# Performance work log

Hardware: AMD Instinct MI355X
Metric: run time of the kernel (lower is better)

Reference implementation:

```python
import jax, jax.numpy as jnp
import numpy as np

NUM_NODES = 64      # nodes per graph (fixed, required by flatten/matricize)
B = 256             # number of graphs
N = B * NUM_NODES   # total nodes
DEG = 16            # out-degree per node
E = N * DEG         # total edges
IN_C, OUT_C, HEADS, EDGE_DIM = 128, 64, 4, 16
NEG_SLOPE = 0.2     # PyG GATv2 leaky_relu slope


def setup_inputs() -> dict:
    key = jax.random.key(0)
    ks = jax.random.split(key, 10)
    x = jax.random.normal(ks[0], (N, IN_C), jnp.float32)
    # within-graph random edges: each node has DEG incoming edges
    dst = jnp.repeat(jnp.arange(N), DEG)
    src = (dst // NUM_NODES) * NUM_NODES + jax.random.randint(ks[1], (E,), 0, NUM_NODES)
    edge_index = jnp.stack([src, dst]).astype(jnp.int64)
    edge_attr = jax.random.normal(ks[2], (E, EDGE_DIM), jnp.float32)
    batch = (jnp.arange(N) // NUM_NODES).astype(jnp.int64)
    s = 0.1
    W_l = jax.random.normal(ks[3], (IN_C, HEADS * OUT_C), jnp.float32) * s
    W_r = jax.random.normal(ks[4], (IN_C, HEADS * OUT_C), jnp.float32) * s
    W_e = jax.random.normal(ks[5], (EDGE_DIM, HEADS * OUT_C), jnp.float32) * s
    att = jax.random.normal(ks[6], (HEADS, OUT_C), jnp.float32) * s
    b_gat = jax.random.normal(ks[7], (HEADS * OUT_C,), jnp.float32) * s
    lin_W = jax.random.normal(ks[8], (NUM_NODES * HEADS * OUT_C, NUM_NODES * OUT_C), jnp.float32) * 0.02
    lin_b = jax.random.normal(ks[9], (NUM_NODES * OUT_C,), jnp.float32) * 0.02
    return {"x": x, "edge_index": edge_index, "edge_attr": edge_attr, "batch": batch,
            "W_l": W_l, "W_r": W_r, "W_e": W_e, "att": att, "b_gat": b_gat,
            "lin_W": lin_W, "lin_b": lin_b}


def _gatv2(x, edge_index, edge_attr, W_l, W_r, W_e, att, b_gat):
    n = x.shape[0]
    src, dst = edge_index[0], edge_index[1]
    # add self loops (PyG default), edge_attr fill_value='mean'
    loop = jnp.arange(n)
    src = jnp.concatenate([src, loop])
    dst = jnp.concatenate([dst, loop])
    mean_ea = jnp.broadcast_to(edge_attr.mean(0, keepdims=True), (n, edge_attr.shape[1]))
    ea = jnp.concatenate([edge_attr, mean_ea], axis=0)
    H, C = att.shape
    xl = (x @ W_l).reshape(n, H, C)   # source transform
    xr = (x @ W_r).reshape(n, H, C)   # target transform
    ee = (ea @ W_e).reshape(-1, H, C)
    feat = xl[src] + xr[dst] + ee                              # [E+N, H, C]
    logits = jnp.einsum('ehc,hc->eh', jax.nn.leaky_relu(feat, NEG_SLOPE), att)
    # segment softmax over incoming edges of each dst node
    seg_max = jax.ops.segment_max(logits, dst, num_segments=n)
    ex = jnp.exp(logits - seg_max[dst])
    denom = jax.ops.segment_sum(ex, dst, num_segments=n)
    alpha = ex / denom[dst]                                    # [E+N, H]
    msg = alpha[:, :, None] * xl[src]                          # [E+N, H, C]
    summed = jax.ops.segment_sum(msg, dst, num_segments=n)
    # aggr='mean': average the weighted messages over neighbors
    cnt = jax.ops.segment_sum(jnp.ones((dst.shape[0],), x.dtype), dst, num_segments=n)
    out = summed / cnt[:, None, None]
    return out.reshape(n, H * C) + b_gat


def reference(x, edge_index, edge_attr, batch, W_l, W_r, W_e, att, b_gat, lin_W, lin_b):
    h = _gatv2(x, edge_index, edge_attr, W_l, W_r, W_e, att, b_gat)  # [N, H*C]
    # flatten: [B, num_nodes*H*C] (batch is sorted, fixed nodes per graph)
    h = h.reshape(B, NUM_NODES * HEADS * OUT_C)
    y = h @ lin_W + lin_b                                            # [B, num_nodes*C]
    # matricize back to node-major layout
    return y.reshape(-1, OUT_C)                                      # [N, C]
```

## Files before the change

### kernel.cpp

```cpp
#include <hip/hip_runtime.h>
#include <hip/hip_bf16.h>

#define N_NODES   16384
#define DEG       16
#define EDGES     262144
#define HC        256
#define KDIM      16384
#define NEG_SLOPE 0.2f

typedef __attribute__((ext_vector_type(8))) short short8;
typedef __attribute__((ext_vector_type(4))) float floatx4;

static __device__ __forceinline__ unsigned short f2bf(float f) {
    union { __hip_bfloat16 h; unsigned short u; } c;
    c.h = __float2bfloat16(f);
    return c.u;
}
static __device__ __forceinline__ unsigned int packbf2(float lo, float hi) {
    union { __hip_bfloat162 h2; unsigned int u; } c;
    c.h2 = __float22bfloat162_rn(make_float2(lo, hi));
    return c.u;
}

template <int CTRL>
static __device__ __forceinline__ float dpp_add(float v) {
    int x = __builtin_amdgcn_update_dpp(0, __float_as_int(v), CTRL, 0xF, 0xF, true);
    return v + __int_as_float(x);
}

__global__ __launch_bounds__(256) void k_ea_part(const float* __restrict__ ea,
                                                 float* __restrict__ part) {
    __shared__ float s[256];
    int b = blockIdx.x, t = threadIdx.x;
    int col = t & 15, r0 = t >> 4;
    const float* base = ea + (size_t)b * 1024 * 16;
    float acc = 0.f;
    for (int r = r0; r < 1024; r += 16) acc += base[r * 16 + col];
    s[t] = acc; __syncthreads();
    for (int off = 128; off >= 16; off >>= 1) {
        if (t < off) s[t] += s[t + off];
        __syncthreads();
    }
    if (t < 16) part[b * 16 + t] = s[t];
}

__global__ __launch_bounds__(256, 4) void k_attn(const int* __restrict__ ei,
                                                 const float* __restrict__ ea,
                                                 const float* __restrict__ eapart,
                                                 const float* __restrict__ att,
                                                 const float* __restrict__ We,
                                                 const float* __restrict__ x,
                                                 const float* __restrict__ Wl,
                                                 const float* __restrict__ Wr,
                                                 const float* __restrict__ bg,
                                                 unsigned short* __restrict__ hb) {
    __shared__ float xlS[64][68];
    __shared__ float xrS[64][68];
    __shared__ __align__(16) char uni[5376];
    __shared__ float mean[16];
    __shared__ float eeselfS[64];

    float* lgS = (float*)uni;
    unsigned int* srcSu = (unsigned int*)(uni + 4352);
    unsigned int* BsU = (unsigned int*)uni;
    float (*ps)[16] = (float(*)[16])uni;

    int t = threadIdx.x;
    int g = blockIdx.x & 255, h = blockIdx.x >> 8;
    int hc0 = h * 64;

    int wave = t >> 6, lane = t & 63;
    int q = lane >> 4, l15 = lane & 15, lk = lane >> 4;

    {
        int col = t & 15, bgi = t >> 4;
        float a = 0.f;
        #pragma unroll
        for (int i = 0; i < 16; ++i)
            a += eapart[(bgi + i * 16) * 16 + col];
        ps[bgi][col] = a;
        __syncthreads();
        if (t < 16) {
            float m = 0.f;
            #pragma unroll
            for (int i = 0; i < 16; ++i) m += ps[i][t];
            mean[t] = m * (1.f / (float)EDGES);
        }
        __syncthreads();
        if (t < 64) {
            float acc = 0.f;
            #pragma unroll
            for (int d = 0; d < 16; ++d) acc += mean[d] * We[d * 256 + hc0 + t];
            eeselfS[t] = acc;
        }
        __syncthreads();
    }

    {
        int wm = wave;
        const float* xrow = x + ((size_t)(g * 64 + wm * 16 + l15)) * 128 + lk * 8;
        floatx4 accL[4], accR[4];
        #pragma unroll
        for (int i = 0; i < 4; ++i) { accL[i] = (floatx4)(0.f); accR[i] = (floatx4)(0.f); }

        int bkp = t >> 4, bc4 = t & 15;

        for (int k0 = 0; k0 < 128; k0 += 32) {
            float4 xv0 = *(const float4*)(xrow + k0);
            float4 xv1 = *(const float4*)(xrow + k0 + 4);
            union { unsigned int u[4]; short8 v; } aa;
            aa.u[0] = packbf2(xv0.x, xv0.y);
            aa.u[1] = packbf2(xv0.z, xv0.w);
            aa.u[2] = packbf2(xv1.x, xv1.y);
            aa.u[3] = packbf2(xv1.z, xv1.w);
            short8 af = aa.v;

            #pragma unroll
            for (int side = 0; side < 2; ++side) {
                const float* Wsel = side ? Wr : Wl;
                __syncthreads();
                {
                    const float* wp = Wsel + (size_t)(k0 + 2 * bkp) * 256 + hc0 + bc4 * 4;
                    float4 r0 = *(const float4*)wp;
                    float4 r1 = *(const float4*)(wp + 256);
                    BsU[(bc4 * 4 + 0) * 18 + bkp] = packbf2(r0.x, r1.x);
                    BsU[(bc4 * 4 + 1) * 18 + bkp] = packbf2(r0.y, r1.y);
                    BsU[(bc4 * 4 + 2) * 18 + bkp] = packbf2(r0.z, r1.z);
                    BsU[(bc4 * 4 + 3) * 18 + bkp] = packbf2(r0.w, r1.w);
                }
                __syncthreads();
                #pragma unroll
                for (int ni = 0; ni < 4; ++ni) {
                    int nr = ni * 16 + l15;
                    union { uint2 u[2]; short8 v; } bb;
                    bb.u[0] = *(const uint2*)&BsU[nr * 18 + lk * 4];
                    bb.u[1] = *(const uint2*)&BsU[nr * 18 + lk * 4 + 2];
                    if (side == 0)
                        accL[ni] = __builtin_amdgcn_mfma_f32_16x16x32_bf16(af, bb.v, accL[ni], 0, 0, 0);
                    else
                        accR[ni] = __builtin_amdgcn_mfma_f32_16x16x32_bf16(af, bb.v, accR[ni], 0, 0, 0);
                }
            }
        }
        #pragma unroll
        for (int ni = 0; ni < 4; ++ni) {
            #pragma unroll
            for (int r = 0; r < 4; ++r) {
                int node = wm * 16 + lk * 4 + r;
                xlS[node][l15 * 4 + ni] = accL[ni][r];
                xrS[node][l15 * 4 + ni] = accR[ni][r];
            }
        }
    }
    __syncthreads();

    {
        int4 v = *(const int4*)(ei + (size_t)g * 1024 + t * 4);
        srcSu[t] = (unsigned int)(v.x & 63) | ((unsigned int)(v.y & 63) << 8) |
                   ((unsigned int)(v.z & 63) << 16) | ((unsigned int)(v.w & 63) << 24);
    }

    short8 wf[4];
    float  attv[4];
    #pragma unroll
    for (int nt = 0; nt < 4; ++nt) {
        attv[nt] = att[hc0 + nt * 16 + l15];
        if (q < 2) {
            const float* wp = We + (size_t)(q * 8) * 256 + hc0 + nt * 16 + l15;
            float w0 = wp[0*256], w1 = wp[1*256], w2 = wp[2*256], w3 = wp[3*256];
            float w4 = wp[4*256], w5 = wp[5*256], w6 = wp[6*256], w7 = wp[7*256];
            union { unsigned int u[4]; short8 v; } bb;
            bb.u[0] = packbf2(w0, w1);
            bb.u[1] = packbf2(w2, w3);
            bb.u[2] = packbf2(w4, w5);
            bb.u[3] = packbf2(w6, w7);
            wf[nt] = bb.v;
        } else {
            wf[nt] = (short8)0;
        }
    }
    __syncthreads();

    for (int b = wave; b < 16; b += 4) {
        short8 af[4];
        #pragma unroll
        for (int mt = 0; mt < 4; ++mt) {
            if (q < 2) {
                const float* ep = ea + ((size_t)(g * 1024 + b * 64 + mt * 16 + l15)) * 16 + q * 8;
                float4 v0 = *(const float4*)ep;
                float4 v1 = *(const float4*)(ep + 4);
                union { unsigned int u[4]; short8 v; } bb;
                bb.u[0] = packbf2(v0.x, v0.y);
                bb.u[1] = packbf2(v0.z, v0.w);
                bb.u[2] = packbf2(v1.x, v1.y);
                bb.u[3] = packbf2(v1.z, v1.w);
                af[mt] = bb.v;
            } else {
                af[mt] = (short8)0;
            }
        }
        floatx4 acc[4][4];
        #pragma unroll
        for (int mt = 0; mt < 4; ++mt)
            #pragma unroll
            for (int nt = 0; nt < 4; ++nt)
                acc[mt][nt] = __builtin_amdgcn_mfma_f32_16x16x32_bf16(af[mt], wf[nt], (floatx4)(0.f), 0, 0, 0);

        #pragma unroll
        for (int mt = 0; mt < 4; ++mt) {
            float4 xrv = *(const float4*)&xrS[b * 4 + mt][l15 * 4];
            unsigned int sw = srcSu[b * 16 + mt * 4 + q];
            int sr[4] = {(int)(sw & 255), (int)((sw >> 8) & 255),
                         (int)((sw >> 16) & 255), (int)(sw >> 24)};
            float lsum[4];
            #pragma unroll
            for (int r = 0; r < 4; ++r) {
                float4 xlv = *(const float4*)&xlS[sr[r]][l15 * 4];
                float f, acc_sum = 0.f;
                f = acc[mt][0][r] + xlv.x + xrv.x; f = fmaxf(f, NEG_SLOPE * f); acc_sum += f * attv[0];
                f = acc[mt][1][r] + xlv.y + xrv.y; f = fmaxf(f, NEG_SLOPE * f); acc_sum += f * attv[1];
                f = acc[mt][2][r] + xlv.z + xrv.z; f = fmaxf(f, NEG_SLOPE * f); acc_sum += f * attv[2];
                f = acc[mt][3][r] + xlv.w + xrv.w; f = fmaxf(f, NEG_SLOPE * f); acc_sum += f * attv[3];
                lsum[r] = acc_sum;
            }
            #pragma unroll
            for (int r = 0; r < 4; ++r) {
                float v = lsum[r];
                v = dpp_add<0x111>(v);
                v = dpp_add<0x112>(v);
                v = dpp_add<0x114>(v);
                v = dpp_add<0x118>(v);
                if (l15 == 15) lgS[b * 64 + mt * 16 + q * 4 + r] = v;
            }
        }
    }

    {
        int n = wave * 16 + l15;
        float sum = 0.f;
        #pragma unroll
        for (int i = 0; i < 4; ++i) {
            float4 ev = *(const float4*)&eeselfS[q * 16 + i * 4];
            float4 av = *(const float4*)(att + hc0 + q * 16 + i * 4);
            #pragma unroll
            for (int j = 0; j < 4; ++j) {
                int p = (i * 4 + j) * 4 + q;
                float e = (j == 0) ? ev.x : (j == 1) ? ev.y : (j == 2) ? ev.z : ev.w;
                float a = (j == 0) ? av.x : (j == 1) ? av.y : (j == 2) ? av.z : av.w;
                float f = xlS[n][p] + xrS[n][p] + e;
                f = fmaxf(f, NEG_SLOPE * f);
                sum += f * a;
            }
        }
        sum += __shfl_xor(sum, 16);
        sum += __shfl_xor(sum, 32);
        if (q == 0) lgS[1024 + n] = sum;
    }
    __syncthreads();

    if (t < 64) {
        float lg[17];
        #pragma unroll
        for (int j = 0; j < 16; ++j) lg[j] = lgS[t * 16 + j];
        lg[16] = lgS[1024 + t];
        float m = lg[0];
        #pragma unroll
        for (int j = 1; j < 17; ++j) m = fmaxf(m, lg[j]);
        float ex[17], ssum = 0.f;
        #pragma unroll
        for (int j = 0; j < 17; ++j) { ex[j] = __expf(lg[j] - m); ssum += ex[j]; }
        float inv = 1.f / (17.f * ssum);
        #pragma unroll
        for (int j = 0; j < 16; ++j) lgS[t * 16 + j] = ex[j] * inv;
        lgS[1024 + t] = ex[16] * inv;
    }
    __syncthreads();

    {
        int c = lane;
        int pc = (c & 15) * 4 + (c >> 4);
        float bgv = bg[hc0 + c];
        for (int n = wave * 16; n < wave * 16 + 16; ++n) {
            float4 al0 = *(const float4*)&lgS[n * 16];
            float4 al1 = *(const float4*)&lgS[n * 16 + 4];
            float4 al2 = *(const float4*)&lgS[n * 16 + 8];
            float4 al3 = *(const float4*)&lgS[n * 16 + 12];
            unsigned int w0 = srcSu[n * 4 + 0], w1 = srcSu[n * 4 + 1];
            unsigned int w2 = srcSu[n * 4 + 2], w3 = srcSu[n * 4 + 3];
            float a0 = lgS[1024 + n] * xlS[n][pc];
            float a1 = 0.f;
            a0 += al0.x * xlS[w0 & 255][pc];        a1 += al0.y * xlS[(w0 >> 8) & 255][pc];
            a0 += al0.z * xlS[(w0 >> 16) & 255][pc]; a1 += al0.w * xlS[w0 >> 24][pc];
            a0 += al1.x * xlS[w1 & 255][pc];        a1 += al1.y * xlS[(w1 >> 8) & 255][pc];
            a0 += al1.z * xlS[(w1 >> 16) & 255][pc]; a1 += al1.w * xlS[w1 >> 24][pc];
            a0 += al2.x * xlS[w2 & 255][pc];        a1 += al2.y * xlS[(w2 >> 8) & 255][pc];
            a0 += al2.z * xlS[(w2 >> 16) & 255][pc]; a1 += al2.w * xlS[w2 >> 24][pc];
            a0 += al3.x * xlS[w3 & 255][pc];        a1 += al3.y * xlS[(w3 >> 8) & 255][pc];
            a0 += al3.z * xlS[(w3 >> 16) & 255][pc]; a1 += al3.w * xlS[w3 >> 24][pc];
            float val = a0 + a1 + bgv;
            hb[((size_t)(g * 64 + n)) * 256 + hc0 + c] = f2bf(val);
        }
    }
}

__global__ __launch_bounds__(256) void k_gemm(const unsigned short* __restrict__ hb,
                                              const float* __restrict__ W,
                                              float* __restrict__ parts) {
    __shared__ unsigned short As[3][256 * 32];
    __shared__ unsigned int   Bs[2][64][18];

    int t = threadIdx.x;
    int wave = t >> 6, lane = t & 63;
    int l15 = lane & 15, lk = lane >> 4;
    int bid = blockIdx.x;
    int s  = bid & 7;
    int n0 = (bid >> 3) * 64;
    int kbase = s * 2048;

    floatx4 acc[4][4];
    #pragma unroll
    for (int i = 0; i < 4; ++i)
        #pragma unroll
        for (int j = 0; j < 4; ++j)
            acc[i][j] = (floatx4)(0.f);

    int gc = ((lane & 3) - ((lane >> 3) & 3)) & 3;
    const unsigned short* a_src =
        hb + (size_t)(wave * 64 + (lane >> 2)) * KDIM + kbase + gc * 8;
    int ap_off[4];
    #pragma unroll
    for (int mi = 0; mi < 4; ++mi)
        ap_off[mi] = (wave * 64 + mi * 16 + l15) * 32 + (((lk + (l15 >> 1)) & 3) * 8);

    int bkp = t >> 4;
    int bc8 = t & 15;
    const float* b_src = W + (size_t)(kbase + 2 * bkp) * 4096 + n0 + bc8 * 4;

    #define ISSUE_A(step, buf)                                                   \
        {                                                                        \
            const unsigned short* gp_ = a_src + (size_t)(step) * 32;             \
            _Pragma("unroll")                                                    \
            for (int i_ = 0; i_ < 4; ++i_) {                                     \
                __builtin_amdgcn_global_load_lds(                                \
                    (const __attribute__((address_space(1))) unsigned int*)      \
                        (gp_ + (size_t)i_ * 16 * KDIM),                          \
                    (__attribute__((address_space(3))) unsigned int*)            \
                        &As[buf][(wave * 64 + i_ * 16) * 32],                    \
                    16, 0, 0);                                                   \
            }                                                                    \
        }
    #define LOAD_B(step, r0, r1)                                                 \
        {                                                                        \
            const float* wp_ = b_src + (size_t)(step) * 32 * 4096;               \
            r0 = *(const float4*)wp_;                                            \
            r1 = *(const float4*)(wp_ + 4096);                                   \
        }
    #define WRITE_B(buf, r0, r1)                                                 \
        {                                                                        \
            Bs[buf][bc8 * 4 + 0][bkp] = packbf2(r0.x, r1.x);                     \
            Bs[buf][bc8 * 4 + 1][bkp] = packbf2(r0.y, r1.y);                     \
            Bs[buf][bc8 * 4 + 2][bkp] = packbf2(r0.z, r1.z);                     \
            Bs[buf][bc8 * 4 + 3][bkp] = packbf2(r0.w, r1.w);                     \
        }
    #define COMPUTE(abuf, bbuf)                                                  \
        {                                                                        \
            short8 a_[4], b_[4];                                                 \
            _Pragma("unroll")                                                    \
            for (int mi = 0; mi < 4; ++mi)                                       \
                a_[mi] = *(const short8*)&As[abuf][ap_off[mi]];                  \
            _Pragma("unroll")                                                    \
            for (int ni = 0; ni < 4; ++ni) {                                     \
                int nr_ = ni * 16 + l15;                                         \
                union { uint2 u[2]; short8 v; } bb_;                             \
                bb_.u[0] = *(const uint2*)&Bs[bbuf][nr_][lk * 4];                \
                bb_.u[1] = *(const uint2*)&Bs[bbuf][nr_][lk * 4 + 2];            \
                b_[ni] = bb_.v;                                                  \
            }                                                                    \
            __builtin_amdgcn_s_setprio(1);                                       \
            _Pragma("unroll")                                                    \
            for (int mi = 0; mi < 4; ++mi)                                       \
                _Pragma("unroll")                                                \
                for (int ni = 0; ni < 4; ++ni)                                   \
                    acc[mi][ni] = __builtin_amdgcn_mfma_f32_16x16x32_bf16(       \
                        a_[mi], b_[ni], acc[mi][ni], 0, 0, 0);                   \
            __builtin_amdgcn_s_setprio(0);                                       \
        }
    #define VMCNT(n) __builtin_amdgcn_sched_barrier(0);                          \
                     asm volatile("s_waitcnt vmcnt(" #n ")" ::: "memory");       \
                     __builtin_amdgcn_sched_barrier(0)
    #define LGKM0    asm volatile("s_waitcnt lgkmcnt(0)" ::: "memory");          \
                     __builtin_amdgcn_sched_barrier(0)
    #define STEP(jA, abufI, jB, ldS0, ldS1, cA, cB, wB, wS0, wS1, VM)            \
        ISSUE_A(jA, abufI);                                                      \
        LOAD_B(jB, ldS0, ldS1);                                                  \
        COMPUTE(cA, cB);                                                         \
        VMCNT(VM);                                                               \
        WRITE_B(wB, wS0, wS1);                                                   \
        LGKM0;                                                                   \
        __builtin_amdgcn_s_barrier();

    float4 s0a, s0b, s1a, s1b, s2a, s2b;

    ISSUE_A(0, 0);
    LOAD_B(0, s0a, s0b);
    ISSUE_A(1, 1);
    LOAD_B(1, s1a, s1b);
    LOAD_B(2, s2a, s2b);
    VMCNT(8);
    WRITE_B(0, s0a, s0b);
    LGKM0;
    __builtin_amdgcn_s_barrier();

    for (int j = 0; j < 60; j += 6) {
        STEP(j + 2, 2, j + 3, s0a, s0b, 0, 0, 1, s1a, s1b, 8)
        STEP(j + 3, 0, j + 4, s1a, s1b, 1, 1, 0, s2a, s2b, 8)
        STEP(j + 4, 1, j + 5, s2a, s2b, 2, 0, 1, s0a, s0b, 8)
        STEP(j + 5, 2, j + 6, s0a, s0b, 0, 1, 0, s1a, s1b, 8)
        STEP(j + 6, 0, j + 7, s1a, s1b, 1, 0, 1, s2a, s2b, 8)
        STEP(j + 7, 1, j + 8, s2a, s2b, 2, 1, 0, s0a, s0b, 8)
    }
    STEP(62, 2, 63, s0a, s0b, 0, 0, 1, s1a, s1b, 8)
    ISSUE_A(63, 0);
    COMPUTE(1, 1);
    VMCNT(6);
    WRITE_B(0, s2a, s2b);
    LGKM0;
    __builtin_amdgcn_s_barrier();
    COMPUTE(2, 0);
    VMCNT(4);
    WRITE_B(1, s0a, s0b);
    LGKM0;
    __builtin_amdgcn_s_barrier();
    VMCNT(0);
    COMPUTE(0, 1);

    #undef ISSUE_A
    #undef LOAD_B
    #undef WRITE_B
    #undef COMPUTE
    #undef VMCNT
    #undef LGKM0
    #undef STEP

    float* dst = parts + (size_t)s * (256 * 4096);
    #pragma unroll
    for (int mi = 0; mi < 4; ++mi) {
        #pragma unroll
        for (int ni = 0; ni < 4; ++ni) {
            int col = n0 + ni * 16 + l15;
            #pragma unroll
            for (int r = 0; r < 4; ++r) {
                int row = wave * 64 + mi * 16 + lk * 4 + r;
                __builtin_nontemporal_store(acc[mi][ni][r],
                                            &dst[(size_t)row * 4096 + col]);
            }
        }
    }
}

__global__ __launch_bounds__(256) void k_reduce(const float* __restrict__ parts,
                                                const float* __restrict__ linb,
                                                float* __restrict__ out) {
    int idx = blockIdx.x * 256 + threadIdx.x;
    float v = linb[idx & 4095];
    #pragma unroll
    for (int s = 0; s < 8; ++s)
        v += __builtin_nontemporal_load(&parts[(size_t)s * (256 * 4096) + idx]);
    __builtin_nontemporal_store(v, &out[idx]);
}

extern "C" void kernel_launch(void* const* d_in, const int* in_sizes, int n_in,
                              void* d_out, int out_size, void* d_ws, size_t ws_size,
                              hipStream_t stream) {
    (void)in_sizes; (void)n_in; (void)out_size; (void)ws_size;
    const float* x   = (const float*)d_in[0];
    const int*   ei  = (const int*)d_in[1];
    const float* ea  = (const float*)d_in[2];
    const float* Wl  = (const float*)d_in[4];
    const float* Wr  = (const float*)d_in[5];
    const float* We  = (const float*)d_in[6];
    const float* att = (const float*)d_in[7];
    const float* bg  = (const float*)d_in[8];
    const float* W   = (const float*)d_in[9];
    const float* lb  = (const float*)d_in[10];
    float* out = (float*)d_out;

    char* p = (char*)d_ws;
    unsigned short* hb  = (unsigned short*)p; p += 8388608;
    float* parts        = (float*)p;          p += 33554432;
    float* eapart       = (float*)p;          p += 16384;

    k_ea_part<<<256,  256, 0, stream>>>(ea, eapart);
    k_attn   <<<1024, 256, 0, stream>>>(ei, ea, eapart, att, We, x, Wl, Wr, bg, hb);
    k_gemm   <<<512,  256, 0, stream>>>(hb, W, parts);
    k_reduce <<<4096, 256, 0, stream>>>(parts, lb, out);
}
```

Baseline: 157.9 us.

## Shrink GEMM A staging to two buffers and reorder compute before loads

The k_gemm kernel's A-tile LDS staging drops from a triple buffer to a double buffer, and launch bounds now request three blocks per CU so more workgroups can be resident. Each pipeline step now runs the MFMA compute on the current buffer before issuing the next A and B global loads into the buffer just freed. The epilogue is remapped to match. This gives up one stage of prefetch depth, so memory latency is less hidden within each block, in exchange for higher occupancy. The af rename in the attention kernel is cosmetic.

```diff
diff --git a/kernel.cpp b/kernel.cpp
--- a/kernel.cpp
+++ b/kernel.cpp
@@ -182,7 +182,7 @@
     __syncthreads();
 
     for (int b = wave; b < 16; b += 4) {
-        short8 af[4];
+        short8 af2[4];
         #pragma unroll
         for (int mt = 0; mt < 4; ++mt) {
             if (q < 2) {
@@ -194,9 +194,9 @@
                 bb.u[1] = packbf2(v0.z, v0.w);
                 bb.u[2] = packbf2(v1.x, v1.y);
                 bb.u[3] = packbf2(v1.z, v1.w);
-                af[mt] = bb.v;
+                af2[mt] = bb.v;
             } else {
-                af[mt] = (short8)0;
+                af2[mt] = (short8)0;
             }
         }
         floatx4 acc[4][4];
@@ -204,7 +204,7 @@
         for (int mt = 0; mt < 4; ++mt)
             #pragma unroll
             for (int nt = 0; nt < 4; ++nt)
-                acc[mt][nt] = __builtin_amdgcn_mfma_f32_16x16x32_bf16(af[mt], wf[nt], (floatx4)(0.f), 0, 0, 0);
+                acc[mt][nt] = __builtin_amdgcn_mfma_f32_16x16x32_bf16(af2[mt], wf[nt], (floatx4)(0.f), 0, 0, 0);
 
         #pragma unroll
         for (int mt = 0; mt < 4; ++mt) {
@@ -303,10 +303,10 @@
     }
 }
 
-__global__ __launch_bounds__(256) void k_gemm(const unsigned short* __restrict__ hb,
-                                              const float* __restrict__ W,
-                                              float* __restrict__ parts) {
-    __shared__ unsigned short As[3][256 * 32];
+__global__ __launch_bounds__(256, 3) void k_gemm(const unsigned short* __restrict__ hb,
+                                                 const float* __restrict__ W,
+                                                 float* __restrict__ parts) {
+    __shared__ unsigned short As[2][256 * 32];
     __shared__ unsigned int   Bs[2][64][18];
 
     int t = threadIdx.x;
@@ -390,10 +390,10 @@
                      __builtin_amdgcn_sched_barrier(0)
     #define LGKM0    asm volatile("s_waitcnt lgkmcnt(0)" ::: "memory");          \
                      __builtin_amdgcn_sched_barrier(0)
-    #define STEP(jA, abufI, jB, ldS0, ldS1, cA, cB, wB, wS0, wS1, VM)            \
-        ISSUE_A(jA, abufI);                                                      \
+    #define STEP(cAB, jA, aBuf, jB, ldS0, ldS1, wB, wS0, wS1, VM)                \
+        COMPUTE(cAB, cAB);                                                       \
+        ISSUE_A(jA, aBuf);                                                       \
         LOAD_B(jB, ldS0, ldS1);                                                  \
-        COMPUTE(cA, cB);                                                         \
         VMCNT(VM);                                                               \
         WRITE_B(wB, wS0, wS1);                                                   \
         LGKM0;                                                                   \
@@ -403,8 +403,8 @@
 
     ISSUE_A(0, 0);
     LOAD_B(0, s0a, s0b);
+    LOAD_B(1, s1a, s1b);
     ISSUE_A(1, 1);
-    LOAD_B(1, s1a, s1b);
     LOAD_B(2, s2a, s2b);
     VMCNT(8);
     WRITE_B(0, s0a, s0b);
@@ -412,27 +412,27 @@
     __builtin_amdgcn_s_barrier();
 
     for (int j = 0; j < 60; j += 6) {
-        STEP(j + 2, 2, j + 3, s0a, s0b, 0, 0, 1, s1a, s1b, 8)
-        STEP(j + 3, 0, j + 4, s1a, s1b, 1, 1, 0, s2a, s2b, 8)
-        STEP(j + 4, 1, j + 5, s2a, s2b, 2, 0, 1, s0a, s0b, 8)
-        STEP(j + 5, 2, j + 6, s0a, s0b, 0, 1, 0, s1a, s1b, 8)
-        STEP(j + 6, 0, j + 7, s1a, s1b, 1, 0, 1, s2a, s2b, 8)
-        STEP(j + 7, 1, j + 8, s2a, s2b, 2, 1, 0, s0a, s0b, 8)
-    }
-    STEP(62, 2, 63, s0a, s0b, 0, 0, 1, s1a, s1b, 8)
-    ISSUE_A(63, 0);
+        STEP(0, j + 2, 0, j + 3, s0a, s0b, 1, s1a, s1b, 8)
+        STEP(1, j + 3, 1, j + 4, s1a, s1b, 0, s2a, s2b, 8)
+        STEP(0, j + 4, 0, j + 5, s2a, s2b, 1, s0a, s0b, 8)
+        STEP(1, j + 5, 1, j + 6, s0a, s0b, 0, s1a, s1b, 8)
+        STEP(0, j + 6, 0, j + 7, s1a, s1b, 1, s2a, s2b, 8)
+        STEP(1, j + 7, 1, j + 8, s2a, s2b, 0, s0a, s0b, 8)
+    }
+    STEP(0, 62, 0, 63, s0a, s0b, 1, s1a, s1b, 8)
     COMPUTE(1, 1);
+    ISSUE_A(63, 1);
     VMCNT(6);
     WRITE_B(0, s2a, s2b);
     LGKM0;
     __builtin_amdgcn_s_barrier();
-    COMPUTE(2, 0);
+    COMPUTE(0, 0);
     VMCNT(4);
     WRITE_B(1, s0a, s0b);
     LGKM0;
     __builtin_amdgcn_s_barrier();
     VMCNT(0);
-    COMPUTE(0, 1);
+    COMPUTE(1, 1);
 
     #undef ISSUE_A
     #undef LOAD_B
```

After: 186.2 us. +17.9%, slower.
